# Kernel optimization log

Hardware: AMD Instinct MI355X
Metric: run time of the kernel (lower is better)

Reference implementation:

```python
import jax, jax.numpy as jnp
import numpy as np

SEQ_LEN = 96      # args.seq_len (in_feats)
H_FEATS = 100
OUT_FEATS = 128
HEADS = 4
K = 64            # args.input_size = nodes per graph
B = 256           # number of graphs (batch_size)
N = K * B
DEG = 8
E = N * DEG
OUT_SIZE = 24     # args.output_size
NEG_SLOPE = 0.2   # PyG GATConv default


def setup_inputs() -> dict:
    key = jax.random.key(0)
    ks = jax.random.split(key, 20)
    s = 0.05
    x = jax.random.normal(ks[0], (N, SEQ_LEN), jnp.float32)
    # intra-graph random edges (dst repeated, src within same graph)
    dst = jnp.repeat(jnp.arange(N, dtype=jnp.int32), DEG)
    src = (dst // K) * K + jax.random.randint(ks[1], (E,), 0, K, dtype=jnp.int32)
    edge_index = jnp.stack([src, dst])
    batch = jnp.repeat(jnp.arange(B, dtype=jnp.int32), K)
    y = jax.random.normal(ks[2], (N, OUT_SIZE), jnp.float32)
    # GATConv 1: in=96 -> heads=4, ch=100
    W1 = jax.random.normal(ks[3], (SEQ_LEN, HEADS * H_FEATS), jnp.float32) * s
    as1 = jax.random.normal(ks[4], (HEADS, H_FEATS), jnp.float32) * s
    ad1 = jax.random.normal(ks[5], (HEADS, H_FEATS), jnp.float32) * s
    b1 = jnp.zeros((H_FEATS,), jnp.float32)
    # GATConv 2: in=100 -> heads=4, ch=128
    W2 = jax.random.normal(ks[6], (H_FEATS, HEADS * OUT_FEATS), jnp.float32) * s
    as2 = jax.random.normal(ks[7], (HEADS, OUT_FEATS), jnp.float32) * s
    ad2 = jax.random.normal(ks[8], (HEADS, OUT_FEATS), jnp.float32) * s
    b2 = jnp.zeros((OUT_FEATS,), jnp.float32)
    # per-node-index MLPs (batched over K)
    fw1 = jax.random.normal(ks[9], (K, OUT_FEATS, 64), jnp.float32) * s
    fb1 = jnp.zeros((K, 64), jnp.float32)
    fw2 = jax.random.normal(ks[10], (K, 64, OUT_SIZE), jnp.float32) * s
    fb2 = jnp.zeros((K, OUT_SIZE), jnp.float32)
    return dict(x=x, edge_index=edge_index, batch=batch, y=y,
                W1=W1, as1=as1, ad1=ad1, b1=b1,
                W2=W2, as2=as2, ad2=ad2, b2=b2,
                fw1=fw1, fb1=fb1, fw2=fw2, fb2=fb2)


def gat_conv(x, src, dst, W, a_src, a_dst, bias):
    # PyG GATConv (concat=False): linear -> per-edge attention -> softmax over
    # incoming edges of each dst -> weighted sum -> mean over heads + bias.
    n = x.shape[0]
    xl = (x @ W).reshape(n, HEADS, -1)                      # [N,H,C]
    al_src = jnp.sum(xl * a_src, axis=-1)                   # [N,H]
    al_dst = jnp.sum(xl * a_dst, axis=-1)                   # [N,H]
    alpha = jax.nn.leaky_relu(al_src[src] + al_dst[dst], NEG_SLOPE)  # [E,H]
    m = jax.ops.segment_max(alpha, dst, num_segments=n)
    ea = jnp.exp(alpha - m[dst])
    denom = jax.ops.segment_sum(ea, dst, num_segments=n)
    w = ea / (denom[dst] + 1e-16)                           # [E,H]
    msg = xl[src] * w[:, :, None]                           # [E,H,C]
    out = jax.ops.segment_sum(msg, dst, num_segments=n)     # [N,H,C]
    return out.mean(axis=1) + bias                          # concat=False


def reference(x, edge_index, batch, y, W1, as1, ad1, b1, W2, as2, ad2, b2, fw1, fb1, fw2, fb2):
    n = x.shape[0]
    src, dst = edge_index[0], edge_index[1]
    loop = jnp.arange(n, dtype=src.dtype)                   # GATConv adds self-loops
    src = jnp.concatenate([src, loop])
    dst = jnp.concatenate([dst, loop])
    h = jax.nn.elu(gat_conv(x, src, dst, W1, as1, ad1, b1))
    h = gat_conv(h, src, dst, W2, as2, ad2, b2)             # [N,128]
    # batch is sorted with K nodes per graph -> stacking == static reshape
    xg = h.reshape(B, K, OUT_FEATS).transpose(1, 0, 2)      # [K,B,128]
    hid = jax.nn.relu(jnp.einsum('kbi,kih->kbh', xg, fw1) + fb1[:, None, :])
    pred = jnp.einsum('kbh,kho->kbo', hid, fw2) + fb2[:, None, :]  # [K,B,out]
    yg = y.reshape(B, K, OUT_SIZE)                          # [B,K,out]
    return pred, yg
```

## Files before the change

### kernel.cpp

```cpp
#include <hip/hip_runtime.h>
#include <hip/hip_bf16.h>
#include <math.h>


#define N_NODES 16384
#define B_GRAPHS 256
#define K_NODES 64
#define DEG 8
#define NHEADS 4
#define C1 100
#define C2 128
#define IN_F 96
#define HID 64
#define OUT_SZ 24
#define PRED_ELEMS (K_NODES * B_GRAPHS * OUT_SZ)

#define W1T_ROWS 448
#define W1T_K    96
#define W2T_ROWS 512
#define W2T_K    128

#define P1N (W1T_ROWS * W1T_K)
#define P2N (W2T_ROWS * W2T_K)
#define F1N (K_NODES * HID * C2)
#define F2N (K_NODES * 32 * HID)
#define YG4 (PRED_ELEMS / 4)
#define WAN (768 + 1024)
#define PREPN (P1N + P2N + F1N + F2N + YG4 + WAN)

using bf16 = __hip_bfloat16;
typedef __attribute__((ext_vector_type(8))) short          frag_ab;
typedef __attribute__((ext_vector_type(4))) float          frag_cd;
typedef unsigned short us8 __attribute__((ext_vector_type(8)));
typedef unsigned short us4 __attribute__((ext_vector_type(4)));

__device__ __forceinline__ float us2f(unsigned short u) {
  return __bfloat162float(__ushort_as_bfloat16(u));
}
__device__ __forceinline__ short f2bf_s(float f) {
  return __builtin_bit_cast(short, __float2bfloat16(f));
}

__global__ __launch_bounds__(256)
void prep(const float* __restrict__ W1, const float* __restrict__ W2,
          const float* __restrict__ fw1, const float* __restrict__ fw2,
          const float* __restrict__ y,
          const float* __restrict__ as1, const float* __restrict__ ad1,
          const float* __restrict__ as2, const float* __restrict__ ad2,
          bf16* __restrict__ W1t, bf16* __restrict__ W2t,
          bf16* __restrict__ fw1t, bf16* __restrict__ fw2t,
          float* __restrict__ yg,
          float* __restrict__ wa1s, float* __restrict__ wa1d,
          float* __restrict__ wa2s, float* __restrict__ wa2d) {
  int idx = blockIdx.x * 256 + threadIdx.x;
  if (idx < P1N) {
    int c = idx / W1T_K, k = idx - c * W1T_K;
    W1t[idx] = __float2bfloat16((c < 400) ? W1[(size_t)k * 400 + c] : 0.f);
  } else if (idx < P1N + P2N) {
    int i2 = idx - P1N;
    int c = i2 >> 7, k = i2 & 127;
    W2t[i2] = __float2bfloat16((k < 100) ? W2[(size_t)k * 512 + c] : 0.f);
  } else if (idx < P1N + P2N + F1N) {
    int i2 = idx - P1N - P2N;
    int k = i2 >> 13, r = i2 & 8191, j = r >> 7, i = r & 127;
    fw1t[i2] = __float2bfloat16(fw1[(size_t)k * 8192 + i * 64 + j]);
  } else if (idx < P1N + P2N + F1N + F2N) {
    int i2 = idx - P1N - P2N - F1N;
    int k = i2 >> 11, r = i2 & 2047, q = r >> 6, j = r & 63;
    fw2t[i2] = __float2bfloat16((q < OUT_SZ) ? fw2[(size_t)k * 1536 + j * 24 + q] : 0.f);
  } else if (idx < P1N + P2N + F1N + F2N + YG4) {
    int j = idx - P1N - P2N - F1N - F2N;
    int i = j * 4;
    float4 v = *(const float4*)(y + i);
    v.x = __bfloat162float(__float2bfloat16(v.x));
    v.y = __bfloat162float(__float2bfloat16(v.y));
    v.z = __bfloat162float(__float2bfloat16(v.z));
    v.w = __bfloat162float(__float2bfloat16(v.w));
    *(float4*)(yg + i) = v;
  } else {
    int tw = idx - P1N - P2N - F1N - F2N - YG4;
    if (tw < 768) {
      int k = tw >> 3, h = (tw >> 1) & 3, sd = tw & 1;
      const float* a = sd ? ad1 : as1;
      float s = 0.f;
      for (int c = 0; c < C1; ++c)
        s += W1[(size_t)k * 400 + h * C1 + c] * a[h * C1 + c];
      (sd ? wa1d : wa1s)[k * 4 + h] = s;
    } else if (tw < WAN) {
      int t2 = tw - 768;
      int k = t2 >> 3, h = (t2 >> 1) & 3, sd = t2 & 1;
      float s = 0.f;
      if (k < 100) {
        const float* a = sd ? ad2 : as2;
        for (int c = 0; c < C2; ++c)
          s += W2[(size_t)k * 512 + h * C2 + c] * a[h * C2 + c];
      }
      (sd ? wa2d : wa2s)[k * 4 + h] = s;
    }
  }
}

__global__ __launch_bounds__(512)
void gat_fused(const float* __restrict__ x,
               const bf16* __restrict__ W1t, const bf16* __restrict__ W2t,
               const int* __restrict__ esrc,
               const float* __restrict__ wa1s_g, const float* __restrict__ wa1d_g,
               const float* __restrict__ wa2s_g, const float* __restrict__ wa2d_g,
               const float* __restrict__ b1, const float* __restrict__ b2,
               bf16* __restrict__ h2out) {
  constexpr int LDA1 = IN_F + 8;
  constexpr int LDA2 = 136;
  constexpr int LDT  = 72;

  __shared__ __align__(16) short          As[64 * LDA2];
  __shared__ __align__(16) unsigned short xs[512 * LDT];
  __shared__ __align__(16) short          Ps[NHEADS * 64 * LDT];
  __shared__ float wa1s[384], wa1d[384], wa2s[512], wa2d[512];
  __shared__ float bia1[C1], bia2[C2];
  __shared__ int   edg[K_NODES * DEG];
  __shared__ float als[64 * 5], ald[64 * 5];

  const int g = blockIdx.x;
  const int t = threadIdx.x;
  const int wv = t >> 6;
  const int l  = t & 63;
  const int lm = l & 15;
  const int lk = (l >> 4) * 8;
  const int rq = (l >> 4) * 4;

  {
    constexpr int QR = IN_F / 4;
    for (int idx = t; idx < 64 * QR; idx += 512) {
      int m = idx / QR, q = idx - m * QR;
      const float4 v = *(const float4*)(x + ((size_t)(g * 64 + m) * IN_F + q * 4));
      short* d = &As[m * LDA1 + q * 4];
      d[0] = f2bf_s(v.x); d[1] = f2bf_s(v.y); d[2] = f2bf_s(v.z); d[3] = f2bf_s(v.w);
    }
  }
  if (t < 384) { wa1s[t] = wa1s_g[t]; wa1d[t] = wa1d_g[t]; }
  { wa2s[t] = wa2s_g[t]; wa2d[t] = wa2d_g[t]; }
  if (t < C1) bia1[t] = b1[t];
  if (t >= 128 && t < 128 + C2) bia2[t - 128] = b2[t - 128];
  edg[t] = esrc[g * K_NODES * DEG + t] & (K_NODES - 1);
  for (int idx = t; idx < NHEADS * 64 * LDT / 8; idx += 512)
    *(us8*)&Ps[idx * 8] = (us8)0;
  __syncthreads();

  if (wv < 7) {
    const int n0 = wv * 64;
    frag_cd acc[4][4] = {};
#pragma unroll
    for (int ks = 0; ks < IN_F; ks += 32) {
      frag_ab b[4];
#pragma unroll
      for (int nt = 0; nt < 4; ++nt)
        b[nt] = *(const frag_ab*)((const short*)W1t +
                                  (size_t)(n0 + nt * 16 + lm) * W1T_K + ks + lk);
#pragma unroll
      for (int mt = 0; mt < 4; ++mt) {
        frag_ab a = *(const frag_ab*)&As[(mt * 16 + lm) * LDA1 + ks + lk];
#pragma unroll
        for (int nt = 0; nt < 4; ++nt)
          acc[mt][nt] = __builtin_amdgcn_mfma_f32_16x16x32_bf16(a, b[nt],
                                                                acc[mt][nt], 0, 0, 0);
      }
    }
#pragma unroll
    for (int mt = 0; mt < 4; ++mt)
#pragma unroll
      for (int nt = 0; nt < 4; ++nt) {
        const int c4 = n0 + nt * 16 + lm;
        us4 o;
#pragma unroll
        for (int r = 0; r < 4; ++r) o[r] = (unsigned short)f2bf_s(acc[mt][nt][r]);
        *(us4*)&xs[c4 * LDT + mt * 16 + rq] = o;
      }
  } else {
    const int n = l;
    float ss[4] = {}, dd[4] = {};
#pragma unroll
    for (int o = 0; o < IN_F / 8; ++o) {
      const us8 v = *(const us8*)&((const unsigned short*)As)[n * LDA1 + o * 8];
#pragma unroll
      for (int j = 0; j < 8; ++j) {
        const float f = us2f(v[j]);
        const int k4 = (o * 8 + j) * 4;
#pragma unroll
        for (int h = 0; h < 4; ++h) {
          ss[h] += f * wa1s[k4 + h];
          dd[h] += f * wa1d[k4 + h];
        }
      }
    }
#pragma unroll
    for (int h = 0; h < 4; ++h) { als[n * 5 + h] = ss[h]; ald[n * 5 + h] = dd[h]; }
  }
  __syncthreads();

  {
    const int mw = (wv & 3) * 16;
    {
      const int n = mw + (l >> 2), h = l & 3;
      const float ad = ald[n * 5 + h];
      int   sv[9];
      float a[9];
#pragma unroll
      for (int j = 0; j < 8; ++j) sv[j] = edg[n * DEG + j];
      sv[8] = n;
#pragma unroll
      for (int j = 0; j < 9; ++j) {
        float v = als[sv[j] * 5 + h] + ad;
        a[j] = (v >= 0.f) ? v : 0.2f * v;
      }
      float m = -1e30f;
#pragma unroll
      for (int j = 0; j < 9; ++j) m = fmaxf(m, a[j]);
      float s = 0.f;
#pragma unroll
      for (int j = 0; j < 9; ++j) { a[j] = __expf(a[j] - m); s += a[j]; }
      const float inv = 1.f / (s + 1e-16f);
      short* prow = &Ps[(h * 64 + n) * LDT];
#pragma unroll
      for (int j = 0; j < 9; ++j) {
        float tw = a[j];
#pragma unroll
        for (int i = 0; i < 9; ++i)
          if (i != j && sv[i] == sv[j]) tw += a[i];
        prow[sv[j]] = f2bf_s(tw * inv);
      }
    }
    if (wv >= 4) {
      for (int i = (wv - 4) * 64 + l; i < 64 * 28; i += 256) {
        int m = i / 28, kk = 100 + (i - m * 28);
        As[m * LDA2 + kk] = 0;
      }
    }
    const int cgi = wv >> 2;
    const int ntb = cgi * 4;
    const int nte = (cgi == 0) ? 4 : 7;
    frag_cd acc[4] = {};
#pragma unroll
    for (int h = 0; h < NHEADS; ++h)
#pragma unroll
      for (int ks = 0; ks < 64; ks += 32) {
        frag_ab a = *(const frag_ab*)&Ps[(h * 64 + mw + lm) * LDT + ks + lk];
        for (int nt = ntb; nt < nte; ++nt) {
          frag_ab b = *(const frag_ab*)&xs[(h * C1 + nt * 16 + lm) * LDT + ks + lk];
          acc[nt - ntb] = __builtin_amdgcn_mfma_f32_16x16x32_bf16(a, b,
                                                                  acc[nt - ntb], 0, 0, 0);
        }
      }
    for (int nt = ntb; nt < nte; ++nt) {
      const int c = nt * 16 + lm;
      if (c < C1) {
        const float bc = bia1[c];
#pragma unroll
        for (int r = 0; r < 4; ++r) {
          float vv = acc[nt - ntb][r] * 0.25f + bc;
          vv = (vv > 0.f) ? vv : (__expf(vv) - 1.f);
          As[(mw + rq + r) * LDA2 + c] = f2bf_s(vv);
        }
      }
    }
  }
  __syncthreads();

  {
    const int n0 = wv * 64;
    frag_cd acc[4][4] = {};
#pragma unroll
    for (int ks = 0; ks < 128; ks += 32) {
      frag_ab b[4];
#pragma unroll
      for (int nt = 0; nt < 4; ++nt)
        b[nt] = *(const frag_ab*)((const short*)W2t +
                                  (size_t)(n0 + nt * 16 + lm) * W2T_K + ks + lk);
#pragma unroll
      for (int mt = 0; mt < 4; ++mt) {
        frag_ab a = *(const frag_ab*)&As[(mt * 16 + lm) * LDA2 + ks + lk];
#pragma unroll
        for (int nt = 0; nt < 4; ++nt)
          acc[mt][nt] = __builtin_amdgcn_mfma_f32_16x16x32_bf16(a, b[nt],
                                                                acc[mt][nt], 0, 0, 0);
      }
    }
#pragma unroll
    for (int mt = 0; mt < 4; ++mt)
#pragma unroll
      for (int nt = 0; nt < 4; ++nt) {
        const int c4 = n0 + nt * 16 + lm;
        us4 o;
#pragma unroll
        for (int r = 0; r < 4; ++r) o[r] = (unsigned short)f2bf_s(acc[mt][nt][r]);
        *(us4*)&xs[c4 * LDT + mt * 16 + rq] = o;
      }
    const int n  = wv * 8 + (l >> 3);
    const int h  = (l >> 1) & 3;
    const int sd = l & 1;
    const float* wa = sd ? wa2d : wa2s;
    float s = 0.f;
#pragma unroll
    for (int o = 0; o < 16; ++o) {
      const us8 v = *(const us8*)&((const unsigned short*)As)[n * LDA2 + o * 8];
#pragma unroll
      for (int j = 0; j < 8; ++j)
        s += us2f(v[j]) * wa[(o * 8 + j) * 4 + h];
    }
    if (sd) ald[n * 5 + h] = s; else als[n * 5 + h] = s;
  }
  __syncthreads();

  {
    const int mw = (wv & 3) * 16;
    {
      const int n = mw + (l >> 2), h = l & 3;
      const float ad = ald[n * 5 + h];
      int   sv[9];
      float a[9];
#pragma unroll
      for (int j = 0; j < 8; ++j) sv[j] = edg[n * DEG + j];
      sv[8] = n;
#pragma unroll
      for (int j = 0; j < 9; ++j) {
        float v = als[sv[j] * 5 + h] + ad;
        a[j] = (v >= 0.f) ? v : 0.2f * v;
      }
      float m = -1e30f;
#pragma unroll
      for (int j = 0; j < 9; ++j) m = fmaxf(m, a[j]);
      float s = 0.f;
#pragma unroll
      for (int j = 0; j < 9; ++j) { a[j] = __expf(a[j] - m); s += a[j]; }
      const float inv = 1.f / (s + 1e-16f);
      short* prow = &Ps[(h * 64 + n) * LDT];
#pragma unroll
      for (int j = 0; j < 9; ++j) {
        float tw = a[j];
#pragma unroll
        for (int i = 0; i < 9; ++i)
          if (i != j && sv[i] == sv[j]) tw += a[i];
        prow[sv[j]] = f2bf_s(tw * inv);
      }
    }
    const int cgi = wv >> 2;
    const int ntb = cgi * 4;
    frag_cd acc[4] = {};
#pragma unroll
    for (int h = 0; h < NHEADS; ++h)
#pragma unroll
      for (int ks = 0; ks < 64; ks += 32) {
        frag_ab a = *(const frag_ab*)&Ps[(h * 64 + mw + lm) * LDT + ks + lk];
#pragma unroll
        for (int nt = 0; nt < 4; ++nt) {
          frag_ab b = *(const frag_ab*)&xs[(h * C2 + (ntb + nt) * 16 + lm) * LDT + ks + lk];
          acc[nt] = __builtin_amdgcn_mfma_f32_16x16x32_bf16(a, b, acc[nt], 0, 0, 0);
        }
      }
    unsigned short* outp = (unsigned short*)h2out + (size_t)(g * 64) * C2;
#pragma unroll
    for (int nt = 0; nt < 4; ++nt) {
      const int c = (ntb + nt) * 16 + lm;
      const float bc = bia2[c];
#pragma unroll
      for (int r = 0; r < 4; ++r) {
        float vv = acc[nt][r] * 0.25f + bc;
        outp[(size_t)(mw + rq + r) * C2 + c] = (unsigned short)f2bf_s(vv);
      }
    }
  }
}

__global__ __launch_bounds__(256)
void mlp_mfma(const bf16* __restrict__ h2,
              const bf16* __restrict__ fw1t, const float* __restrict__ fb1,
              const bf16* __restrict__ fw2t, const float* __restrict__ fb2,
              float* __restrict__ pred) {
  constexpr int LDA = 136;
  constexpr int LDH = 72;
  __shared__ __align__(16) short As[32 * LDA];
  __shared__ __align__(16) short B1[HID * LDA];
  __shared__ __align__(16) short Hs[32 * LDH];
  __shared__ __align__(16) short B2[32 * LDH];
  __shared__ float b1s[HID];
  __shared__ float b2s[32];

  const int k  = blockIdx.x & 63;
  const int ms = blockIdx.x >> 6;
  const int t  = threadIdx.x;

  for (int idx = t; idx < 32 * 16; idx += 256) {
    int r = idx >> 4, o = idx & 15;
    const us8 v = *(const us8*)((const unsigned short*)h2 +
        ((size_t)((ms * 32 + r) * K_NODES + k) * C2) + o * 8);
    *(us8*)&As[r * LDA + o * 8] = v;
  }
  for (int idx = t; idx < HID * 16; idx += 256) {
    int n = idx >> 4, o = idx & 15;
    *(us8*)&B1[n * LDA + o * 8] =
        *(const us8*)((const unsigned short*)fw1t + (size_t)k * 8192 + n * 128 + o * 8);
  }
  for (int idx = t; idx < 32 * 8; idx += 256) {
    int q = idx >> 3, o = idx & 7;
    *(us8*)&B2[q * LDH + o * 8] =
        *(const us8*)((const unsigned short*)fw2t + (size_t)k * 2048 + q * 64 + o * 8);
  }
  if (t < HID) b1s[t] = fb1[k * HID + t];
  if (t >= 64 && t < 96) b2s[t - 64] = (t - 64 < OUT_SZ) ? fb2[k * OUT_SZ + (t - 64)] : 0.f;
  __syncthreads();

  const int wv = t >> 6;
  const int l  = t & 63;
  const int lm = l & 15;
  const int lk = (l >> 4) * 8;
  const int rq = (l >> 4) * 4;

  {
    const int mt  = wv & 1;
    const int ntp = wv >> 1;
    frag_cd acc[2] = {};
#pragma unroll
    for (int ks = 0; ks < C2; ks += 32) {
      frag_ab a = *(const frag_ab*)&As[(mt * 16 + lm) * LDA + ks + lk];
#pragma unroll
      for (int u = 0; u < 2; ++u) {
        frag_ab b = *(const frag_ab*)&B1[((ntp * 2 + u) * 16 + lm) * LDA + ks + lk];
        acc[u] = __builtin_amdgcn_mfma_f32_16x16x32_bf16(a, b, acc[u], 0, 0, 0);
      }
    }
#pragma unroll
    for (int u = 0; u < 2; ++u) {
      const int j  = (ntp * 2 + u) * 16 + lm;
      const float bj = b1s[j];
#pragma unroll
      for (int r = 0; r < 4; ++r)
        Hs[(mt * 16 + rq + r) * LDH + j] = f2bf_s(fmaxf(acc[u][r] + bj, 0.f));
    }
  }
  __syncthreads();

  {
    const int mt = wv >> 1;
    const int nt = wv & 1;
    frag_cd acc = {};
#pragma unroll
    for (int ks = 0; ks < HID; ks += 32) {
      frag_ab a = *(const frag_ab*)&Hs[(mt * 16 + lm) * LDH + ks + lk];
      frag_ab b = *(const frag_ab*)&B2[(nt * 16 + lm) * LDH + ks + lk];
      acc = __builtin_amdgcn_mfma_f32_16x16x32_bf16(a, b, acc, 0, 0, 0);
    }
    const int q = nt * 16 + lm;
    if (q < OUT_SZ) {
      const float bq = b2s[q];
#pragma unroll
      for (int r = 0; r < 4; ++r)
        pred[((size_t)k * B_GRAPHS + ms * 32 + mt * 16 + rq + r) * OUT_SZ + q] = acc[r] + bq;
    }
  }
}

extern "C" void kernel_launch(void* const* d_in, const int* in_sizes, int n_in,
                              void* d_out, int out_size, void* d_ws, size_t ws_size,
                              hipStream_t stream) {
  const float* x   = (const float*)d_in[0];
  const int*   ei  = (const int*)d_in[1];
  const float* y   = (const float*)d_in[3];
  const float* W1  = (const float*)d_in[4];
  const float* as1 = (const float*)d_in[5];
  const float* ad1 = (const float*)d_in[6];
  const float* b1  = (const float*)d_in[7];
  const float* W2  = (const float*)d_in[8];
  const float* as2 = (const float*)d_in[9];
  const float* ad2 = (const float*)d_in[10];
  const float* b2  = (const float*)d_in[11];
  const float* fw1 = (const float*)d_in[12];
  const float* fb1 = (const float*)d_in[13];
  const float* fw2 = (const float*)d_in[14];
  const float* fb2 = (const float*)d_in[15];

  bf16* h2    = (bf16*)d_ws;
  bf16* W1t   = h2 + (size_t)N_NODES * C2;
  bf16* W2t   = W1t + P1N;
  bf16* fw1t  = W2t + P2N;
  bf16* fw2t  = fw1t + F1N;
  float* wa1s = (float*)(fw2t + F2N);
  float* wa1d = wa1s + 384;
  float* wa2s = wa1d + 384;
  float* wa2d = wa2s + 512;

  float* out = (float*)d_out;

  prep<<<(PREPN + 255) / 256, 256, 0, stream>>>(
      W1, W2, fw1, fw2, y, as1, ad1, as2, ad2,
      W1t, W2t, fw1t, fw2t, out + PRED_ELEMS, wa1s, wa1d, wa2s, wa2d);

  gat_fused<<<B_GRAPHS, 512, 0, stream>>>(x, W1t, W2t, ei,
                                          wa1s, wa1d, wa2s, wa2d, b1, b2, h2);

  mlp_mfma<<<K_NODES * 8, 256, 0, stream>>>(h2, fw1t, fb1, fw2t, fb2, out);
}
```

Before: 123.1 us.

## Split fused GAT kernel into two per-layer kernels partitioned by head pairs

The single per-graph fused GAT kernel (256 blocks of 512 threads) is replaced by two kernels, one per GAT layer. Each launches 512 blocks of 256 threads, and each block handles one graph and two of the four heads. Each half writes partial head sums to global memory in bf16. The next stage adds the two halves, applying bias and ELU for layer 1 and a plain sum for layer 2 before the MLP. This is meant to raise occupancy and block count on the GPU, at the cost of an extra launch, extra global round-trips of the intermediates, duplicated input loads, and an extra bf16 rounding step.

```diff
diff --git a/kernel.cpp b/kernel.cpp
--- a/kernel.cpp
+++ b/kernel.cpp
@@ -100,54 +100,46 @@
   }
 }
 
-__global__ __launch_bounds__(512)
-void gat_fused(const float* __restrict__ x,
-               const bf16* __restrict__ W1t, const bf16* __restrict__ W2t,
-               const int* __restrict__ esrc,
-               const float* __restrict__ wa1s_g, const float* __restrict__ wa1d_g,
-               const float* __restrict__ wa2s_g, const float* __restrict__ wa2d_g,
-               const float* __restrict__ b1, const float* __restrict__ b2,
-               bf16* __restrict__ h2out) {
-  constexpr int LDA1 = IN_F + 8;
-  constexpr int LDA2 = 136;
-  constexpr int LDT  = 72;
-
-  __shared__ __align__(16) short          As[64 * LDA2];
-  __shared__ __align__(16) unsigned short xs[512 * LDT];
-  __shared__ __align__(16) short          Ps[NHEADS * 64 * LDT];
-  __shared__ float wa1s[384], wa1d[384], wa2s[512], wa2d[512];
-  __shared__ float bia1[C1], bia2[C2];
+__global__ __launch_bounds__(256)
+void gat1(const float* __restrict__ x, const bf16* __restrict__ W1t,
+          const int* __restrict__ esrc,
+          const float* __restrict__ wa1s_g, const float* __restrict__ wa1d_g,
+          bf16* __restrict__ h1p) {
+  constexpr int LDA = IN_F + 8;
+  constexpr int LDT = 72;
+  __shared__ __align__(16) short          As[64 * LDA];
+  __shared__ __align__(16) unsigned short xs[256 * LDT];
+  __shared__ __align__(16) short          Ps[2 * 64 * LDT];
+  __shared__ float wls[96 * 2], wld[96 * 2];
   __shared__ int   edg[K_NODES * DEG];
-  __shared__ float als[64 * 5], ald[64 * 5];
-
-  const int g = blockIdx.x;
+  __shared__ float als[64 * 3], ald[64 * 3];
+
+  const int g    = blockIdx.x >> 1;
+  const int half = blockIdx.x & 1;
   const int t = threadIdx.x;
-  const int wv = t >> 6;
-  const int l  = t & 63;
-  const int lm = l & 15;
-  const int lk = (l >> 4) * 8;
-  const int rq = (l >> 4) * 4;
-
-  {
-    constexpr int QR = IN_F / 4;
-    for (int idx = t; idx < 64 * QR; idx += 512) {
-      int m = idx / QR, q = idx - m * QR;
-      const float4 v = *(const float4*)(x + ((size_t)(g * 64 + m) * IN_F + q * 4));
-      short* d = &As[m * LDA1 + q * 4];
-      d[0] = f2bf_s(v.x); d[1] = f2bf_s(v.y); d[2] = f2bf_s(v.z); d[3] = f2bf_s(v.w);
-    }
-  }
-  if (t < 384) { wa1s[t] = wa1s_g[t]; wa1d[t] = wa1d_g[t]; }
-  { wa2s[t] = wa2s_g[t]; wa2d[t] = wa2d_g[t]; }
-  if (t < C1) bia1[t] = b1[t];
-  if (t >= 128 && t < 128 + C2) bia2[t - 128] = b2[t - 128];
-  edg[t] = esrc[g * K_NODES * DEG + t] & (K_NODES - 1);
-  for (int idx = t; idx < NHEADS * 64 * LDT / 8; idx += 512)
+  const int wv = t >> 6, l = t & 63, lm = l & 15;
+  const int lk = (l >> 4) * 8, rq = (l >> 4) * 4;
+
+  for (int idx = t; idx < 64 * 24; idx += 256) {
+    int m = idx / 24, q = idx - m * 24;
+    const float4 v = *(const float4*)(x + ((size_t)(g * 64 + m) * IN_F + q * 4));
+    short* d = &As[m * LDA + q * 4];
+    d[0] = f2bf_s(v.x); d[1] = f2bf_s(v.y); d[2] = f2bf_s(v.z); d[3] = f2bf_s(v.w);
+  }
+  if (t < 192) {
+    int k = t >> 1, h = t & 1;
+    wls[t] = wa1s_g[k * 4 + half * 2 + h];
+    wld[t] = wa1d_g[k * 4 + half * 2 + h];
+  }
+  for (int idx = t; idx < K_NODES * DEG; idx += 256)
+    edg[idx] = esrc[g * K_NODES * DEG + idx] & (K_NODES - 1);
+  for (int idx = t; idx < 2 * 64 * LDT / 8; idx += 256)
     *(us8*)&Ps[idx * 8] = (us8)0;
   __syncthreads();
 
-  if (wv < 7) {
-    const int n0 = wv * 64;
+  {
+    const int cg = half * 3 + wv;
+    const int n0 = cg * 64;
     frag_cd acc[4][4] = {};
 #pragma unroll
     for (int ks = 0; ks < IN_F; ks += 32) {
@@ -158,7 +150,7 @@
                                   (size_t)(n0 + nt * 16 + lm) * W1T_K + ks + lk);
 #pragma unroll
       for (int mt = 0; mt < 4; ++mt) {
-        frag_ab a = *(const frag_ab*)&As[(mt * 16 + lm) * LDA1 + ks + lk];
+        frag_ab a = *(const frag_ab*)&As[(mt * 16 + lm) * LDA + ks + lk];
 #pragma unroll
         for (int nt = 0; nt < 4; ++nt)
           acc[mt][nt] = __builtin_amdgcn_mfma_f32_16x16x32_bf16(a, b[nt],
@@ -169,47 +161,36 @@
     for (int mt = 0; mt < 4; ++mt)
 #pragma unroll
       for (int nt = 0; nt < 4; ++nt) {
-        const int c4 = n0 + nt * 16 + lm;
         us4 o;
 #pragma unroll
         for (int r = 0; r < 4; ++r) o[r] = (unsigned short)f2bf_s(acc[mt][nt][r]);
-        *(us4*)&xs[c4 * LDT + mt * 16 + rq] = o;
-      }
-  } else {
-    const int n = l;
-    float ss[4] = {}, dd[4] = {};
-#pragma unroll
-    for (int o = 0; o < IN_F / 8; ++o) {
-      const us8 v = *(const us8*)&((const unsigned short*)As)[n * LDA1 + o * 8];
-#pragma unroll
-      for (int j = 0; j < 8; ++j) {
-        const float f = us2f(v[j]);
-        const int k4 = (o * 8 + j) * 4;
-#pragma unroll
-        for (int h = 0; h < 4; ++h) {
-          ss[h] += f * wa1s[k4 + h];
-          dd[h] += f * wa1d[k4 + h];
-        }
-      }
-    }
-#pragma unroll
-    for (int h = 0; h < 4; ++h) { als[n * 5 + h] = ss[h]; ald[n * 5 + h] = dd[h]; }
+        *(us4*)&xs[(wv * 64 + nt * 16 + lm) * LDT + mt * 16 + rq] = o;
+      }
+    const int n = t & 63, h = (t >> 6) & 1, sd = t >> 7;
+    const float* w = sd ? wld : wls;
+    float s = 0.f;
+#pragma unroll
+    for (int o = 0; o < 12; ++o) {
+      const us8 v = *(const us8*)&((const unsigned short*)As)[n * LDA + o * 8];
+#pragma unroll
+      for (int j = 0; j < 8; ++j) s += us2f(v[j]) * w[(o * 8 + j) * 2 + h];
+    }
+    (sd ? ald : als)[n * 3 + h] = s;
   }
   __syncthreads();
 
   {
-    const int mw = (wv & 3) * 16;
-    {
-      const int n = mw + (l >> 2), h = l & 3;
-      const float ad = ald[n * 5 + h];
-      int   sv[9];
-      float a[9];
+    const int mw = wv * 16;
+    if (l < 32) {
+      const int n = mw + (l >> 1), h = l & 1;
+      const float ad = ald[n * 3 + h];
+      int sv[9]; float a[9];
 #pragma unroll
       for (int j = 0; j < 8; ++j) sv[j] = edg[n * DEG + j];
       sv[8] = n;
 #pragma unroll
       for (int j = 0; j < 9; ++j) {
-        float v = als[sv[j] * 5 + h] + ad;
+        float v = als[sv[j] * 3 + h] + ad;
         a[j] = (v >= 0.f) ? v : 0.2f * v;
       }
       float m = -1e30f;
@@ -229,44 +210,92 @@
         prow[sv[j]] = f2bf_s(tw * inv);
       }
     }
-    if (wv >= 4) {
-      for (int i = (wv - 4) * 64 + l; i < 64 * 28; i += 256) {
-        int m = i / 28, kk = 100 + (i - m * 28);
-        As[m * LDA2 + kk] = 0;
-      }
-    }
-    const int cgi = wv >> 2;
-    const int ntb = cgi * 4;
-    const int nte = (cgi == 0) ? 4 : 7;
-    frag_cd acc[4] = {};
-#pragma unroll
-    for (int h = 0; h < NHEADS; ++h)
+    frag_cd acc[7] = {};
+#pragma unroll
+    for (int hh = 0; hh < 2; ++hh) {
+      const int lb = (half ? 8 : 0) + hh * C1;
 #pragma unroll
       for (int ks = 0; ks < 64; ks += 32) {
-        frag_ab a = *(const frag_ab*)&Ps[(h * 64 + mw + lm) * LDT + ks + lk];
-        for (int nt = ntb; nt < nte; ++nt) {
-          frag_ab b = *(const frag_ab*)&xs[(h * C1 + nt * 16 + lm) * LDT + ks + lk];
-          acc[nt - ntb] = __builtin_amdgcn_mfma_f32_16x16x32_bf16(a, b,
-                                                                  acc[nt - ntb], 0, 0, 0);
+        frag_ab a = *(const frag_ab*)&Ps[(hh * 64 + mw + lm) * LDT + ks + lk];
+#pragma unroll
+        for (int nt = 0; nt < 7; ++nt) {
+          frag_ab b = *(const frag_ab*)&xs[(lb + nt * 16 + lm) * LDT + ks + lk];
+          acc[nt] = __builtin_amdgcn_mfma_f32_16x16x32_bf16(a, b, acc[nt], 0, 0, 0);
         }
       }
-    for (int nt = ntb; nt < nte; ++nt) {
+    }
+    bf16* outp = h1p + (size_t)half * N_NODES * C1 + (size_t)(g * 64) * C1;
+#pragma unroll
+    for (int nt = 0; nt < 7; ++nt) {
       const int c = nt * 16 + lm;
       if (c < C1) {
-        const float bc = bia1[c];
-#pragma unroll
-        for (int r = 0; r < 4; ++r) {
-          float vv = acc[nt - ntb][r] * 0.25f + bc;
-          vv = (vv > 0.f) ? vv : (__expf(vv) - 1.f);
-          As[(mw + rq + r) * LDA2 + c] = f2bf_s(vv);
-        }
-      }
-    }
-  }
+#pragma unroll
+        for (int r = 0; r < 4; ++r)
+          outp[(size_t)(mw + rq + r) * C1 + c] = __float2bfloat16(acc[nt][r]);
+      }
+    }
+  }
+}
+
+__global__ __launch_bounds__(256)
+void gat2(const bf16* __restrict__ h1p, const bf16* __restrict__ W2t,
+          const int* __restrict__ esrc,
+          const float* __restrict__ wa2s_g, const float* __restrict__ wa2d_g,
+          const float* __restrict__ b1, const float* __restrict__ b2,
+          bf16* __restrict__ h2p) {
+  constexpr int LDA = 136;
+  constexpr int LDT = 72;
+  __shared__ __align__(16) short          As[64 * LDA];
+  __shared__ __align__(16) unsigned short xs[256 * LDT];
+  __shared__ __align__(16) short          Ps[2 * 64 * LDT];
+  __shared__ float wls[128 * 2], wld[128 * 2];
+  __shared__ float bia2[C2];
+  __shared__ int   edg[K_NODES * DEG];
+  __shared__ float als[64 * 3], ald[64 * 3];
+
+  const int g    = blockIdx.x >> 1;
+  const int half = blockIdx.x & 1;
+  const int t = threadIdx.x;
+  const int wv = t >> 6, l = t & 63, lm = l & 15;
+  const int lk = (l >> 4) * 8, rq = (l >> 4) * 4;
+
+  {
+    const bf16* p0 = h1p + (size_t)(g * 64) * C1;
+    const bf16* p1 = h1p + (size_t)N_NODES * C1 + (size_t)(g * 64) * C1;
+    for (int idx = t; idx < 64 * 25; idx += 256) {
+      int n = idx / 25, q = (idx - n * 25) * 4;
+      const us4 a = *(const us4*)((const unsigned short*)p0 + (size_t)n * C1 + q);
+      const us4 b = *(const us4*)((const unsigned short*)p1 + (size_t)n * C1 + q);
+      const float4 bb = *(const float4*)(b1 + q);
+      const float bv[4] = {bb.x, bb.y, bb.z, bb.w};
+      short* d = &As[n * LDA + q];
+#pragma unroll
+      for (int j = 0; j < 4; ++j) {
+        float v = 0.25f * (us2f(a[j]) + us2f(b[j])) + bv[j];
+        v = (v > 0.f) ? v : (__expf(v) - 1.f);
+        d[j] = f2bf_s(v);
+      }
+    }
+    for (int idx = t; idx < 64 * 28; idx += 256) {
+      int m = idx / 28, kk = 100 + (idx - m * 28);
+      As[m * LDA + kk] = 0;
+    }
+  }
+  {
+    int k = t >> 1, h = t & 1;
+    wls[t] = wa2s_g[k * 4 + half * 2 + h];
+    wld[t] = wa2d_g[k * 4 + half * 2 + h];
+  }
+  if (t < C2) bia2[t] = b2[t];
+  for (int idx = t; idx < K_NODES * DEG; idx += 256)
+    edg[idx] = esrc[g * K_NODES * DEG + idx] & (K_NODES - 1);
+  for (int idx = t; idx < 2 * 64 * LDT / 8; idx += 256)
+    *(us8*)&Ps[idx * 8] = (us8)0;
   __syncthreads();
 
   {
-    const int n0 = wv * 64;
+    const int cg = half * 4 + wv;
+    const int n0 = cg * 64;
     frag_cd acc[4][4] = {};
 #pragma unroll
     for (int ks = 0; ks < 128; ks += 32) {
@@ -277,7 +306,7 @@
                                   (size_t)(n0 + nt * 16 + lm) * W2T_K + ks + lk);
 #pragma unroll
       for (int mt = 0; mt < 4; ++mt) {
-        frag_ab a = *(const frag_ab*)&As[(mt * 16 + lm) * LDA2 + ks + lk];
+        frag_ab a = *(const frag_ab*)&As[(mt * 16 + lm) * LDA + ks + lk];
 #pragma unroll
         for (int nt = 0; nt < 4; ++nt)
           acc[mt][nt] = __builtin_amdgcn_mfma_f32_16x16x32_bf16(a, b[nt],
@@ -288,41 +317,36 @@
     for (int mt = 0; mt < 4; ++mt)
 #pragma unroll
       for (int nt = 0; nt < 4; ++nt) {
-        const int c4 = n0 + nt * 16 + lm;
         us4 o;
 #pragma unroll
         for (int r = 0; r < 4; ++r) o[r] = (unsigned short)f2bf_s(acc[mt][nt][r]);
-        *(us4*)&xs[c4 * LDT + mt * 16 + rq] = o;
-      }
-    const int n  = wv * 8 + (l >> 3);
-    const int h  = (l >> 1) & 3;
-    const int sd = l & 1;
-    const float* wa = sd ? wa2d : wa2s;
+        *(us4*)&xs[(wv * 64 + nt * 16 + lm) * LDT + mt * 16 + rq] = o;
+      }
+    const int n = t & 63, h = (t >> 6) & 1, sd = t >> 7;
+    const float* w = sd ? wld : wls;
     float s = 0.f;
 #pragma unroll
     for (int o = 0; o < 16; ++o) {
-      const us8 v = *(const us8*)&((const unsigned short*)As)[n * LDA2 + o * 8];
-#pragma unroll
-      for (int j = 0; j < 8; ++j)
-        s += us2f(v[j]) * wa[(o * 8 + j) * 4 + h];
-    }
-    if (sd) ald[n * 5 + h] = s; else als[n * 5 + h] = s;
+      const us8 v = *(const us8*)&((const unsigned short*)As)[n * LDA + o * 8];
+#pragma unroll
+      for (int j = 0; j < 8; ++j) s += us2f(v[j]) * w[(o * 8 + j) * 2 + h];
+    }
+    (sd ? ald : als)[n * 3 + h] = s;
   }
   __syncthreads();
 
   {
-    const int mw = (wv & 3) * 16;
-    {
-      const int n = mw + (l >> 2), h = l & 3;
-      const float ad = ald[n * 5 + h];
-      int   sv[9];
-      float a[9];
+    const int mw = wv * 16;
+    if (l < 32) {
+      const int n = mw + (l >> 1), h = l & 1;
+      const float ad = ald[n * 3 + h];
+      int sv[9]; float a[9];
 #pragma unroll
       for (int j = 0; j < 8; ++j) sv[j] = edg[n * DEG + j];
       sv[8] = n;
 #pragma unroll
       for (int j = 0; j < 9; ++j) {
-        float v = als[sv[j] * 5 + h] + ad;
+        float v = als[sv[j] * 3 + h] + ad;
         a[j] = (v >= 0.f) ? v : 0.2f * v;
       }
       float m = -1e30f;
@@ -342,36 +366,34 @@
         prow[sv[j]] = f2bf_s(tw * inv);
       }
     }
-    const int cgi = wv >> 2;
-    const int ntb = cgi * 4;
-    frag_cd acc[4] = {};
-#pragma unroll
-    for (int h = 0; h < NHEADS; ++h)
+    frag_cd acc[8] = {};
+#pragma unroll
+    for (int hh = 0; hh < 2; ++hh) {
+      const int lb = hh * C2;
 #pragma unroll
       for (int ks = 0; ks < 64; ks += 32) {
-        frag_ab a = *(const frag_ab*)&Ps[(h * 64 + mw + lm) * LDT + ks + lk];
-#pragma unroll
-        for (int nt = 0; nt < 4; ++nt) {
-          frag_ab b = *(const frag_ab*)&xs[(h * C2 + (ntb + nt) * 16 + lm) * LDT + ks + lk];
+        frag_ab a = *(const frag_ab*)&Ps[(hh * 64 + mw + lm) * LDT + ks + lk];
+#pragma unroll
+        for (int nt = 0; nt < 8; ++nt) {
+          frag_ab b = *(const frag_ab*)&xs[(lb + nt * 16 + lm) * LDT + ks + lk];
           acc[nt] = __builtin_amdgcn_mfma_f32_16x16x32_bf16(a, b, acc[nt], 0, 0, 0);
         }
       }
-    unsigned short* outp = (unsigned short*)h2out + (size_t)(g * 64) * C2;
-#pragma unroll
-    for (int nt = 0; nt < 4; ++nt) {
-      const int c = (ntb + nt) * 16 + lm;
-      const float bc = bia2[c];
-#pragma unroll
-      for (int r = 0; r < 4; ++r) {
-        float vv = acc[nt][r] * 0.25f + bc;
-        outp[(size_t)(mw + rq + r) * C2 + c] = (unsigned short)f2bf_s(vv);
-      }
+    }
+    bf16* outp = h2p + (size_t)half * N_NODES * C2 + (size_t)(g * 64) * C2;
+#pragma unroll
+    for (int nt = 0; nt < 8; ++nt) {
+      const int c = nt * 16 + lm;
+      const float bc = half ? 0.f : bia2[c];
+#pragma unroll
+      for (int r = 0; r < 4; ++r)
+        outp[(size_t)(mw + rq + r) * C2 + c] = __float2bfloat16(0.25f * acc[nt][r] + bc);
     }
   }
 }
 
 __global__ __launch_bounds__(256)
-void mlp_mfma(const bf16* __restrict__ h2,
+void mlp_mfma(const bf16* __restrict__ h2p,
               const bf16* __restrict__ fw1t, const float* __restrict__ fb1,
               const bf16* __restrict__ fw2t, const float* __restrict__ fb2,
               float* __restrict__ pred) {
@@ -388,11 +410,18 @@
   const int ms = blockIdx.x >> 6;
   const int t  = threadIdx.x;
 
+  const unsigned short* p0 = (const unsigned short*)h2p;
+  const unsigned short* p1 = p0 + (size_t)N_NODES * C2;
   for (int idx = t; idx < 32 * 16; idx += 256) {
     int r = idx >> 4, o = idx & 15;
-    const us8 v = *(const us8*)((const unsigned short*)h2 +
-        ((size_t)((ms * 32 + r) * K_NODES + k) * C2) + o * 8);
-    *(us8*)&As[r * LDA + o * 8] = v;
+    const size_t off = ((size_t)((ms * 32 + r) * K_NODES + k) * C2) + o * 8;
+    const us8 a = *(const us8*)(p0 + off);
+    const us8 b = *(const us8*)(p1 + off);
+    us8 s;
+#pragma unroll
+    for (int j = 0; j < 8; ++j)
+      s[j] = (unsigned short)f2bf_s(us2f(a[j]) + us2f(b[j]));
+    *(us8*)&As[r * LDA + o * 8] = s;
   }
   for (int idx = t; idx < HID * 16; idx += 256) {
     int n = idx >> 4, o = idx & 15;
@@ -408,11 +437,8 @@
   if (t >= 64 && t < 96) b2s[t - 64] = (t - 64 < OUT_SZ) ? fb2[k * OUT_SZ + (t - 64)] : 0.f;
   __syncthreads();
 
-  const int wv = t >> 6;
-  const int l  = t & 63;
-  const int lm = l & 15;
-  const int lk = (l >> 4) * 8;
-  const int rq = (l >> 4) * 4;
+  const int wv = t >> 6, l = t & 63, lm = l & 15;
+  const int lk = (l >> 4) * 8, rq = (l >> 4) * 4;
 
   {
     const int mt  = wv & 1;
@@ -477,8 +503,9 @@
   const float* fw2 = (const float*)d_in[14];
   const float* fb2 = (const float*)d_in[15];
 
-  bf16* h2    = (bf16*)d_ws;
-  bf16* W1t   = h2 + (size_t)N_NODES * C2;
+  bf16* h1p   = (bf16*)d_ws;
+  bf16* h2p   = h1p + (size_t)2 * N_NODES * C1;
+  bf16* W1t   = h2p + (size_t)2 * N_NODES * C2;
   bf16* W2t   = W1t + P1N;
   bf16* fw1t  = W2t + P2N;
   bf16* fw2t  = fw1t + F1N;
@@ -493,8 +520,8 @@
       W1, W2, fw1, fw2, y, as1, ad1, as2, ad2,
       W1t, W2t, fw1t, fw2t, out + PRED_ELEMS, wa1s, wa1d, wa2s, wa2d);
 
-  gat_fused<<<B_GRAPHS, 512, 0, stream>>>(x, W1t, W2t, ei,
-                                          wa1s, wa1d, wa2s, wa2d, b1, b2, h2);
-
-  mlp_mfma<<<K_NODES * 8, 256, 0, stream>>>(h2, fw1t, fb1, fw2t, fb2, out);
-}
+  gat1<<<B_GRAPHS * 2, 256, 0, stream>>>(x, W1t, ei, wa1s, wa1d, h1p);
+  gat2<<<B_GRAPHS * 2, 256, 0, stream>>>(h1p, W2t, ei, wa2s, wa2d, b1, b2, h2p);
+
+  mlp_mfma<<<K_NODES * 8, 256, 0, stream>>>(h2p, fw1t, fb1, fw2t, fb2, out);
+}
```

Result: slower. 126.1 us (+2.4%).
